# Kernel optimization log

Measured on AMD Instinct MI355X. Metric: run time of the kernel, lower is better.

Reference implementation:

```python
import jax, jax.numpy as jnp
import numpy as np

M, K, N = 8192, 4096, 11008
GS = 128
G = K // GS  # 32 groups along reduction dim


def setup_inputs() -> dict:
    key = jax.random.key(0)
    k1, k2, k3, k4 = jax.random.split(key, 4)
    inp = jax.random.normal(k1, (M, K), dtype=jnp.float32)
    # packed int4 weights: two nibbles per byte along K -> [K//2, N]
    weight = jax.random.randint(k2, (K // 2, N), 0, 256, dtype=jnp.int32)
    scale = jax.random.uniform(k3, (G, N), dtype=jnp.float32)
    zp = jax.random.randint(k4, (G, N), 0, 16, dtype=jnp.int32)
    return {"input": inp, "weight": weight, "scale": scale, "zp": zp, "gs": GS}


def dequant_int4(weight, scale, zp, gs):
    # unpack nibbles: low nibble first, then high -> interleaved along K
    low = weight & 0xF            # [K//2, N]
    high = (weight >> 4) & 0xF    # [K//2, N]
    w = jnp.stack([low, high], axis=1).reshape(weight.shape[0] * 2, weight.shape[1])  # [K, N]
    g = w.shape[0] // gs
    wg = w.reshape(g, gs, w.shape[1])                          # [G, gs, N]
    wd = (wg - zp[:, None, :]).astype(scale.dtype) * scale[:, None, :]
    return wd.reshape(w.shape[0], w.shape[1])                  # [K, N] float


def reference(input, weight, scale, zp, gs):
    W = dequant_int4(weight, scale, zp, gs)      # [K, N]
    return input @ W                             # [M, N]
```

## Files before the change

### kernel.cpp

```cpp
#include <hip/hip_runtime.h>


constexpr int M = 8192;
constexpr int K = 4096;
constexpr int N = 11008;

constexpr int BM = 256;
constexpr int BN = 256;
constexpr int BK = 32;
constexpr int KT = K / BK;

typedef short v8s __attribute__((ext_vector_type(8)));
typedef float v4f __attribute__((ext_vector_type(4)));

__device__ __forceinline__ unsigned pack_bf16(float lo, float hi) {
    unsigned a = __builtin_bit_cast(unsigned, lo);
    a += 0x7FFFu + ((a >> 16) & 1u);
    unsigned b = __builtin_bit_cast(unsigned, hi);
    b += 0x7FFFu + ((b >> 16) & 1u);
    return (a >> 16) | (b & 0xFFFF0000u);
}

constexpr int PREP_A_BLOCKS = (M / 256) * KT * 256 / 256;
constexpr int PREP_B_BLOCKS = (N / 256) * KT * 4 * 256 / 256;

__global__ __launch_bounds__(256) void prep(const float* __restrict__ A,
                                            const int* __restrict__ Wq,
                                            const float* __restrict__ scale,
                                            const int* __restrict__ zp,
                                            uint4* __restrict__ At,
                                            uint4* __restrict__ Bt)
{
    const int tid = threadIdx.x;
    if (blockIdx.x < PREP_A_BLOCKS) {
        const int u  = blockIdx.x * 256 + tid;
        const int r  = u & 255;
        const int kt = (u >> 8) & 127;
        const int mt = u >> 15;
        const float* src = A + (size_t)(mt * 256 + r) * K + kt * 32;
        float4 f[8];
        #pragma unroll
        for (int i = 0; i < 8; ++i)
            f[i] = reinterpret_cast<const float4*>(src)[i];
        const size_t base = (size_t)(mt * KT + kt) * 1024 + r;
        #pragma unroll
        for (int c = 0; c < 4; ++c) {
            uint4 w;
            w.x = pack_bf16(f[2 * c].x, f[2 * c].y);
            w.y = pack_bf16(f[2 * c].z, f[2 * c].w);
            w.z = pack_bf16(f[2 * c + 1].x, f[2 * c + 1].y);
            w.w = pack_bf16(f[2 * c + 1].z, f[2 * c + 1].w);
            At[base + c * 256] = w;
        }
    } else {
        const size_t u = (size_t)(blockIdx.x - PREP_A_BLOCKS) * 256 + tid;
        const int r  = (int)(u & 255);
        const int c  = (int)((u >> 8) & 3);
        const int kt = (int)((u >> 10) & 127);
        const int nt = (int)(u >> 17);
        const int n  = nt * 256 + r;
        const int g  = kt >> 2;
        const float sc = scale[(size_t)g * N + n];
        const float zs = -sc * (float)zp[(size_t)g * N + n];
        const int* src = Wq + (size_t)(kt * 16 + c * 4) * N + n;
        unsigned q0 = (unsigned)src[0];
        unsigned q1 = (unsigned)src[(size_t)N];
        unsigned q2 = (unsigned)src[(size_t)2 * N];
        unsigned q3 = (unsigned)src[(size_t)3 * N];
        uint4 o;
        o.x = pack_bf16(fmaf((float)(q0 & 15u), sc, zs),
                        fmaf((float)((q0 >> 4) & 15u), sc, zs));
        o.y = pack_bf16(fmaf((float)(q1 & 15u), sc, zs),
                        fmaf((float)((q1 >> 4) & 15u), sc, zs));
        o.z = pack_bf16(fmaf((float)(q2 & 15u), sc, zs),
                        fmaf((float)((q2 >> 4) & 15u), sc, zs));
        o.w = pack_bf16(fmaf((float)(q3 & 15u), sc, zs),
                        fmaf((float)((q3 >> 4) & 15u), sc, zs));
        Bt[u] = o;
    }
}


__device__ __forceinline__ void stage_step(const unsigned short* __restrict__ At,
                                           const unsigned short* __restrict__ Bt,
                                           int bx, int by, int t, int buf,
                                           int tid, unsigned short* sMem)
{
    const unsigned short* aT = At + (size_t)(bx * KT + t) * 1024 * 8;
    const unsigned short* bT = Bt + (size_t)(by * KT + t) * 1024 * 8;
    unsigned short* sa = sMem + (size_t)buf * 2048 * 8;
    unsigned short* sb = sa + 1024 * 8;
    #pragma unroll
    for (int i = 0; i < 2; ++i) {
        const int s = i * 512 + tid;
        __builtin_amdgcn_global_load_lds(
            (const __attribute__((address_space(1))) void*)(aT + (size_t)s * 8),
            (__attribute__((address_space(3))) void*)(sa + (size_t)(s & ~63) * 8),
            16, 0, 0);
        __builtin_amdgcn_global_load_lds(
            (const __attribute__((address_space(1))) void*)(bT + (size_t)s * 8),
            (__attribute__((address_space(3))) void*)(sb + (size_t)(s & ~63) * 8),
            16, 0, 0);
    }
}

__device__ __forceinline__ void compute_step(const unsigned short* sMem, int buf,
                                             int wm, int wn, int quad, int l16,
                                             v4f (&acc)[8][4])
{
    const unsigned short* sa = sMem + (size_t)buf * 2048 * 8;
    const unsigned short* sb = sa + 1024 * 8;
    v8s af[8], bfr[4];
    #pragma unroll
    for (int i = 0; i < 8; ++i)
        af[i] = *reinterpret_cast<const v8s*>(&sa[(quad * 256 + wm + i * 16 + l16) * 8]);
    #pragma unroll
    for (int j = 0; j < 4; ++j)
        bfr[j] = *reinterpret_cast<const v8s*>(&sb[(quad * 256 + wn + j * 16 + l16) * 8]);
    __builtin_amdgcn_s_setprio(1);
    #pragma unroll
    for (int i = 0; i < 8; ++i)
        #pragma unroll
        for (int j = 0; j < 4; ++j)
            acc[i][j] = __builtin_amdgcn_mfma_f32_16x16x32_bf16(
                af[i], bfr[j], acc[i][j], 0, 0, 0);
    __builtin_amdgcn_s_setprio(0);
}

__global__ __launch_bounds__(512, 2) void qgemm_bf16(
    const unsigned short* __restrict__ At,
    const unsigned short* __restrict__ Bt,
    float* __restrict__ C)
{
    __shared__ unsigned short sMem[4 * 2048 * 8];

    const int tid  = threadIdx.x;
    const int bx   = blockIdx.x;
    const int by   = blockIdx.y;
    const int lane = tid & 63;
    const int wave = tid >> 6;
    const int wm   = (wave >> 2) * 128;
    const int wn   = (wave & 3) * 64;
    const int l16  = lane & 15;
    const int quad = lane >> 4;

    v4f acc[8][4];
    #pragma unroll
    for (int i = 0; i < 8; ++i)
        #pragma unroll
        for (int j = 0; j < 4; ++j)
            acc[i][j] = (v4f){0.f, 0.f, 0.f, 0.f};

    stage_step(At, Bt, bx, by, 0, 0, tid, sMem);
    stage_step(At, Bt, bx, by, 1, 1, tid, sMem);
    stage_step(At, Bt, bx, by, 2, 2, tid, sMem);

    for (int t = 0; t < KT; ++t) {
        if (t < KT - 2) {
            asm volatile("s_waitcnt vmcnt(8)" ::: "memory");
        } else if (t == KT - 2) {
            asm volatile("s_waitcnt vmcnt(4)" ::: "memory");
        } else {
            asm volatile("s_waitcnt vmcnt(0)" ::: "memory");
        }
        __builtin_amdgcn_s_barrier();
        if (t + 3 < KT)
            stage_step(At, Bt, bx, by, t + 3, (t + 3) & 3, tid, sMem);
        compute_step(sMem, t & 3, wm, wn, quad, l16, acc);
    }

    const int m0 = bx * BM;
    const int n0 = by * BN;
    #pragma unroll
    for (int i = 0; i < 8; ++i) {
        int rbase = m0 + wm + i * 16 + quad * 4;
        #pragma unroll
        for (int j = 0; j < 4; ++j) {
            int col = n0 + wn + j * 16 + l16;
            #pragma unroll
            for (int r = 0; r < 4; ++r)
                C[(size_t)(rbase + r) * N + col] = acc[i][j][r];
        }
    }
}

constexpr int FBM = 128, FBN = 128, FBK = 64;

__global__ __launch_bounds__(256) void qgemm_kernel(
    const float* __restrict__ A,
    const int*   __restrict__ Wq,
    const float* __restrict__ scale,
    const int*   __restrict__ zp,
    float*       __restrict__ C)
{
    __shared__ unsigned short sA[(FBK / 8) * FBM * 8];
    __shared__ unsigned short sB[(FBK / 8) * FBN * 8];

    const int t  = threadIdx.x;
    const int m0 = blockIdx.x * FBM;
    const int n0 = blockIdx.y * FBN;

    const int lane = t & 63;
    const int wave = t >> 6;
    const int wm   = (wave & 1) * 64;
    const int wn   = (wave >> 1) * 64;
    const int l16  = lane & 15;
    const int quad = lane >> 4;

    const int bn  = t & 127;
    const int brg = t >> 7;

    v4f acc[4][4];
    #pragma unroll
    for (int i = 0; i < 4; ++i)
        #pragma unroll
        for (int j = 0; j < 4; ++j)
            acc[i][j] = (v4f){0.f, 0.f, 0.f, 0.f};

    for (int kt = 0; kt < K / FBK; ++kt) {
        const int k0 = kt * FBK;
        const int gq = k0 >> 7;
        const float sc = scale[gq * N + n0 + bn];
        const float zs = -sc * (float)zp[gq * N + n0 + bn];

        __syncthreads();

        #pragma unroll
        for (int p = 0; p < 4; ++p) {
            int idx = t + p * 256;
            int m = idx >> 3;
            int c = idx & 7;
            const float* src = A + (size_t)(m0 + m) * K + k0 + c * 8;
            float4 f0 = *reinterpret_cast<const float4*>(src);
            float4 f1 = *reinterpret_cast<const float4*>(src + 4);
            uint4 w;
            w.x = pack_bf16(f0.x, f0.y);
            w.y = pack_bf16(f0.z, f0.w);
            w.z = pack_bf16(f1.x, f1.y);
            w.w = pack_bf16(f1.z, f1.w);
            *reinterpret_cast<uint4*>(&sA[(c * FBM + m) * 8]) = w;
        }

        #pragma unroll
        for (int p = 0; p < 4; ++p) {
            int g = brg + p * 2;
            const int* src = Wq + (size_t)((k0 >> 1) + g * 4) * N + n0 + bn;
            unsigned q0 = (unsigned)src[0];
            unsigned q1 = (unsigned)src[N];
            unsigned q2 = (unsigned)src[2 * N];
            unsigned q3 = (unsigned)src[3 * N];
            uint4 o;
            o.x = pack_bf16(fmaf((float)(q0 & 15u), sc, zs),
                            fmaf((float)((q0 >> 4) & 15u), sc, zs));
            o.y = pack_bf16(fmaf((float)(q1 & 15u), sc, zs),
                            fmaf((float)((q1 >> 4) & 15u), sc, zs));
            o.z = pack_bf16(fmaf((float)(q2 & 15u), sc, zs),
                            fmaf((float)((q2 >> 4) & 15u), sc, zs));
            o.w = pack_bf16(fmaf((float)(q3 & 15u), sc, zs),
                            fmaf((float)((q3 >> 4) & 15u), sc, zs));
            *reinterpret_cast<uint4*>(&sB[(g * FBN + bn) * 8]) = o;
        }

        __syncthreads();

        #pragma unroll
        for (int kw = 0; kw < 2; ++kw) {
            int cb = kw * 4 + quad;
            v8s af[4], bfr[4];
            #pragma unroll
            for (int i = 0; i < 4; ++i)
                af[i] = *reinterpret_cast<const v8s*>(&sA[(cb * FBM + wm + i * 16 + l16) * 8]);
            #pragma unroll
            for (int j = 0; j < 4; ++j)
                bfr[j] = *reinterpret_cast<const v8s*>(&sB[(cb * FBN + wn + j * 16 + l16) * 8]);
            #pragma unroll
            for (int i = 0; i < 4; ++i)
                #pragma unroll
                for (int j = 0; j < 4; ++j)
                    acc[i][j] = __builtin_amdgcn_mfma_f32_16x16x32_bf16(
                        af[i], bfr[j], acc[i][j], 0, 0, 0);
        }
    }

    #pragma unroll
    for (int i = 0; i < 4; ++i) {
        int rbase = m0 + wm + i * 16 + quad * 4;
        #pragma unroll
        for (int j = 0; j < 4; ++j) {
            int col = n0 + wn + j * 16 + l16;
            #pragma unroll
            for (int r = 0; r < 4; ++r)
                C[(size_t)(rbase + r) * N + col] = acc[i][j][r];
        }
    }
}

extern "C" void kernel_launch(void* const* d_in, const int* in_sizes, int n_in,
                              void* d_out, int out_size, void* d_ws, size_t ws_size,
                              hipStream_t stream) {
    const float* A     = (const float*)d_in[0];
    const int*   Wq    = (const int*)d_in[1];
    const float* scale = (const float*)d_in[2];
    const int*   zp    = (const int*)d_in[3];
    float*       C     = (float*)d_out;

    const size_t needA = (size_t)M * K * 2;
    const size_t needB = (size_t)N * K * 2;

    if (d_ws != nullptr && ws_size >= needA + needB) {
        unsigned short* At = (unsigned short*)d_ws;
        unsigned short* Bt = (unsigned short*)((char*)d_ws + needA);

        prep<<<dim3(PREP_A_BLOCKS + PREP_B_BLOCKS), dim3(256), 0, stream>>>(
            A, Wq, scale, zp, (uint4*)At, (uint4*)Bt);
        qgemm_bf16<<<dim3(M / BM, N / BN), dim3(512), 0, stream>>>(At, Bt, C);
    } else {
        qgemm_kernel<<<dim3(M / FBM, N / FBN), dim3(256), 0, stream>>>(A, Wq, scale, zp, C);
    }
}
```

Before: 1.148 ms.

## Split GEMM main loop into interleaved A/B staging and half-tile MFMA clusters

Restructures the bf16 GEMM main loop into a manually unrolled schedule of four K-steps. Each step issues the A and B global-to-LDS loads separately and splits the 8x4 MFMA block into two 4-row clusters, with barriers placed around them. The goal is to spread memory issue across the compute phases and keep fewer A fragments live at once, in the style of ping-pong scheduling. In exchange it adds many extra workgroup barriers per K-step, and the waitcnt bookkeeping is fragile.

```diff
diff --git a/kernel.cpp b/kernel.cpp
--- a/kernel.cpp
+++ b/kernel.cpp
@@ -12,6 +12,8 @@
 
 typedef short v8s __attribute__((ext_vector_type(8)));
 typedef float v4f __attribute__((ext_vector_type(4)));
+
+#define BAR() asm volatile("s_barrier" ::: "memory")
 
 __device__ __forceinline__ unsigned pack_bf16(float lo, float hi) {
     unsigned a = __builtin_bit_cast(unsigned, lo);
@@ -81,15 +83,12 @@
 }
 
 
-__device__ __forceinline__ void stage_step(const unsigned short* __restrict__ At,
-                                           const unsigned short* __restrict__ Bt,
-                                           int bx, int by, int t, int buf,
-                                           int tid, unsigned short* sMem)
+__device__ __forceinline__ void stage_A(const unsigned short* __restrict__ At,
+                                        int bx, int t, int buf, int tid,
+                                        unsigned short* sMem)
 {
     const unsigned short* aT = At + (size_t)(bx * KT + t) * 1024 * 8;
-    const unsigned short* bT = Bt + (size_t)(by * KT + t) * 1024 * 8;
     unsigned short* sa = sMem + (size_t)buf * 2048 * 8;
-    unsigned short* sb = sa + 1024 * 8;
     #pragma unroll
     for (int i = 0; i < 2; ++i) {
         const int s = i * 512 + tid;
@@ -97,6 +96,18 @@
             (const __attribute__((address_space(1))) void*)(aT + (size_t)s * 8),
             (__attribute__((address_space(3))) void*)(sa + (size_t)(s & ~63) * 8),
             16, 0, 0);
+    }
+}
+
+__device__ __forceinline__ void stage_B(const unsigned short* __restrict__ Bt,
+                                        int by, int t, int buf, int tid,
+                                        unsigned short* sMem)
+{
+    const unsigned short* bT = Bt + (size_t)(by * KT + t) * 1024 * 8;
+    unsigned short* sb = sMem + (size_t)buf * 2048 * 8 + 1024 * 8;
+    #pragma unroll
+    for (int i = 0; i < 2; ++i) {
+        const int s = i * 512 + tid;
         __builtin_amdgcn_global_load_lds(
             (const __attribute__((address_space(1))) void*)(bT + (size_t)s * 8),
             (__attribute__((address_space(3))) void*)(sb + (size_t)(s & ~63) * 8),
@@ -104,26 +115,30 @@
     }
 }
 
-__device__ __forceinline__ void compute_step(const unsigned short* sMem, int buf,
-                                             int wm, int wn, int quad, int l16,
-                                             v4f (&acc)[8][4])
+__device__ __forceinline__ void cluster(const unsigned short* sMem, int buf, int i0,
+                                        int wm, int wn, int quad, int l16,
+                                        v4f (&acc)[8][4], v8s (&bfr)[4])
 {
     const unsigned short* sa = sMem + (size_t)buf * 2048 * 8;
     const unsigned short* sb = sa + 1024 * 8;
-    v8s af[8], bfr[4];
-    #pragma unroll
-    for (int i = 0; i < 8; ++i)
-        af[i] = *reinterpret_cast<const v8s*>(&sa[(quad * 256 + wm + i * 16 + l16) * 8]);
-    #pragma unroll
-    for (int j = 0; j < 4; ++j)
-        bfr[j] = *reinterpret_cast<const v8s*>(&sb[(quad * 256 + wn + j * 16 + l16) * 8]);
+    v8s af[4];
+    if (i0 == 0) {
+        #pragma unroll
+        for (int j = 0; j < 4; ++j)
+            bfr[j] = *reinterpret_cast<const v8s*>(
+                &sb[(quad * 256 + wn + j * 16 + l16) * 8]);
+    }
+    #pragma unroll
+    for (int i = 0; i < 4; ++i)
+        af[i] = *reinterpret_cast<const v8s*>(
+            &sa[(quad * 256 + wm + (i0 + i) * 16 + l16) * 8]);
     __builtin_amdgcn_s_setprio(1);
     #pragma unroll
-    for (int i = 0; i < 8; ++i)
+    for (int i = 0; i < 4; ++i)
         #pragma unroll
         for (int j = 0; j < 4; ++j)
-            acc[i][j] = __builtin_amdgcn_mfma_f32_16x16x32_bf16(
-                af[i], bfr[j], acc[i][j], 0, 0, 0);
+            acc[i0 + i][j] = __builtin_amdgcn_mfma_f32_16x16x32_bf16(
+                af[i], bfr[j], acc[i0 + i][j], 0, 0, 0);
     __builtin_amdgcn_s_setprio(0);
 }
 
@@ -151,22 +166,82 @@
         for (int j = 0; j < 4; ++j)
             acc[i][j] = (v4f){0.f, 0.f, 0.f, 0.f};
 
-    stage_step(At, Bt, bx, by, 0, 0, tid, sMem);
-    stage_step(At, Bt, bx, by, 1, 1, tid, sMem);
-    stage_step(At, Bt, bx, by, 2, 2, tid, sMem);
-
-    for (int t = 0; t < KT; ++t) {
-        if (t < KT - 2) {
-            asm volatile("s_waitcnt vmcnt(8)" ::: "memory");
-        } else if (t == KT - 2) {
-            asm volatile("s_waitcnt vmcnt(4)" ::: "memory");
-        } else {
-            asm volatile("s_waitcnt vmcnt(0)" ::: "memory");
-        }
-        __builtin_amdgcn_s_barrier();
-        if (t + 3 < KT)
-            stage_step(At, Bt, bx, by, t + 3, (t + 3) & 3, tid, sMem);
-        compute_step(sMem, t & 3, wm, wn, quad, l16, acc);
+    stage_A(At, bx, 0, 0, tid, sMem);
+    stage_B(Bt, by, 0, 0, tid, sMem);
+    stage_A(At, bx, 1, 1, tid, sMem);
+    stage_B(Bt, by, 1, 1, tid, sMem);
+    stage_A(At, bx, 2, 2, tid, sMem);
+    stage_B(Bt, by, 2, 2, tid, sMem);
+
+    v8s bfr[4];
+
+    for (int u = 0; u < KT / 4 - 1; ++u) {
+        const int s0 = 4 * u;
+        stage_A(At, bx, s0 + 3, 3, tid, sMem);
+        asm volatile("s_waitcnt vmcnt(10)" ::: "memory");
+        BAR();
+        cluster(sMem, 0, 0, wm, wn, quad, l16, acc, bfr);
+        BAR();
+        stage_B(Bt, by, s0 + 3, 3, tid, sMem);
+        BAR();
+        cluster(sMem, 0, 4, wm, wn, quad, l16, acc, bfr);
+        BAR();
+        stage_A(At, bx, s0 + 4, 0, tid, sMem);
+        asm volatile("s_waitcnt vmcnt(10)" ::: "memory");
+        BAR();
+        cluster(sMem, 1, 0, wm, wn, quad, l16, acc, bfr);
+        BAR();
+        stage_B(Bt, by, s0 + 4, 0, tid, sMem);
+        BAR();
+        cluster(sMem, 1, 4, wm, wn, quad, l16, acc, bfr);
+        BAR();
+        stage_A(At, bx, s0 + 5, 1, tid, sMem);
+        asm volatile("s_waitcnt vmcnt(10)" ::: "memory");
+        BAR();
+        cluster(sMem, 2, 0, wm, wn, quad, l16, acc, bfr);
+        BAR();
+        stage_B(Bt, by, s0 + 5, 1, tid, sMem);
+        BAR();
+        cluster(sMem, 2, 4, wm, wn, quad, l16, acc, bfr);
+        BAR();
+        stage_A(At, bx, s0 + 6, 2, tid, sMem);
+        asm volatile("s_waitcnt vmcnt(10)" ::: "memory");
+        BAR();
+        cluster(sMem, 3, 0, wm, wn, quad, l16, acc, bfr);
+        BAR();
+        stage_B(Bt, by, s0 + 6, 2, tid, sMem);
+        BAR();
+        cluster(sMem, 3, 4, wm, wn, quad, l16, acc, bfr);
+        BAR();
+    }
+
+    {
+        stage_A(At, bx, KT - 1, 3, tid, sMem);
+        asm volatile("s_waitcnt vmcnt(10)" ::: "memory");
+        BAR();
+        cluster(sMem, 0, 0, wm, wn, quad, l16, acc, bfr);
+        BAR();
+        stage_B(Bt, by, KT - 1, 3, tid, sMem);
+        BAR();
+        cluster(sMem, 0, 4, wm, wn, quad, l16, acc, bfr);
+        BAR();
+        asm volatile("s_waitcnt vmcnt(8)" ::: "memory");
+        BAR();
+        cluster(sMem, 1, 0, wm, wn, quad, l16, acc, bfr);
+        BAR();
+        cluster(sMem, 1, 4, wm, wn, quad, l16, acc, bfr);
+        BAR();
+        asm volatile("s_waitcnt vmcnt(4)" ::: "memory");
+        BAR();
+        cluster(sMem, 2, 0, wm, wn, quad, l16, acc, bfr);
+        BAR();
+        cluster(sMem, 2, 4, wm, wn, quad, l16, acc, bfr);
+        BAR();
+        asm volatile("s_waitcnt vmcnt(0)" ::: "memory");
+        BAR();
+        cluster(sMem, 3, 0, wm, wn, quad, l16, acc, bfr);
+        BAR();
+        cluster(sMem, 3, 4, wm, wn, quad, l16, acc, bfr);
     }
 
     const int m0 = bx * BM;
```

Measured after the change: 1.103 ms. 3.9% less time.
